# Performance work log

Hardware: AMD Instinct MI355X
Metric: run time of the kernel (lower is better)

## Reference

```python
import jax, jax.numpy as jnp
import numpy as np

Z, N, D_MODEL, HEADS = 2, 2048, 1024, 16
DK = D_MODEL // HEADS


def setup_inputs() -> dict:
    key = jax.random.key(0)
    ks = jax.random.split(key, 9)
    xavier = (6.0 / (DK + D_MODEL)) ** 0.5
    x = jax.random.normal(ks[0], (Z, N, D_MODEL), jnp.float32)
    mask = jax.random.randint(ks[1], (Z, N), 0, 2) > 0  # bool validity mask
    q_proj = jax.random.uniform(ks[2], (HEADS, D_MODEL, DK), jnp.float32, -xavier, xavier)
    k_proj = jax.random.uniform(ks[3], (HEADS, D_MODEL, DK), jnp.float32, -xavier, xavier)
    v_proj = jax.random.uniform(ks[4], (HEADS, D_MODEL, DK), jnp.float32, -xavier, xavier)
    q_bias = jnp.zeros((HEADS, DK), jnp.float32)
    k_bias = jnp.zeros((HEADS, DK), jnp.float32)
    v_bias = jnp.zeros((HEADS, DK), jnp.float32)
    lim = 1.0 / (D_MODEL ** 0.5)
    out_w = jax.random.uniform(ks[5], (D_MODEL, D_MODEL), jnp.float32, -lim, lim)  # torch Linear weight [out, in]
    return {"x": x, "mask": mask, "q_proj": q_proj, "k_proj": k_proj, "v_proj": v_proj,
            "q_bias": q_bias, "k_bias": k_bias, "v_bias": v_bias, "out_w": out_w}


def reference(x, mask, q_proj, k_proj, v_proj, q_bias, k_bias, v_bias, out_w):
    # Per-head QKV projections: [Z,N,Dm] x [H,Dm,Dk] -> [Z,H,N,Dk]
    Q = jnp.einsum('znd,hdk->zhnk', x, q_proj) + q_bias[None, :, None, :]
    K = jnp.einsum('znd,hdk->zhnk', x, k_proj) + k_bias[None, :, None, :]
    V = jnp.einsum('znd,hdk->zhnk', x, v_proj) + v_bias[None, :, None, :]
    scale = q_proj.shape[-1] ** -0.5
    # Dense equivalent of flash_attn_varlen over valid (unpadded) tokens:
    # mask invalid keys, softmax, then zero outputs at invalid query positions.
    scores = jnp.einsum('zhnk,zhmk->zhnm', Q, K) * scale
    neg = jnp.asarray(-1e9, scores.dtype)
    scores = jnp.where(mask[:, None, None, :], scores, neg)
    attn = jax.nn.softmax(scores, axis=-1)
    ctx = jnp.einsum('zhnm,zhmk->zhnk', attn, V)
    ctx = jnp.where(mask[:, None, :, None], ctx, jnp.zeros((), ctx.dtype))
    z, h, n, dk = ctx.shape
    out = ctx.transpose(0, 2, 1, 3).reshape(z, n, h * dk)  # [Z,N,Dm]
    return out @ out_w.T  # nn.Linear(d_model, d_model, bias=False)
```

## Files before the change

kernel.cpp:

```cpp
#include <hip/hip_runtime.h>
#include <stdint.h>

typedef __bf16 bf16_t;
typedef __bf16 bf16x8 __attribute__((ext_vector_type(8)));
typedef __bf16 bf16x4 __attribute__((ext_vector_type(4)));
typedef float f32x4 __attribute__((ext_vector_type(4)));

#define MFMA16(A, B, C) __builtin_amdgcn_mfma_f32_16x16x32_bf16(A, B, C, 0, 0, 0)

#if __has_builtin(__builtin_amdgcn_exp2f)
#define EXP2F(x) __builtin_amdgcn_exp2f(x)
#else
#define EXP2F(x) exp2f(x)
#endif

#define GLOAD_LDS16(g, l)                                                   \
  __builtin_amdgcn_global_load_lds(                                         \
      (const __attribute__((address_space(1))) void*)(g),                   \
      (__attribute__((address_space(3))) void*)(l), 16, 0, 0)

#define SL2E 0.18033688011112042f
#define VT_STRIDE 131072

__global__ __launch_bounds__(256) void convert_kernel(
    const float* __restrict__ x, const float* __restrict__ qw, const float* __restrict__ kw,
    const float* __restrict__ vw, const float* __restrict__ qb, const float* __restrict__ kb,
    const float* __restrict__ vb, const float* __restrict__ ow,
    bf16_t* __restrict__ xb, bf16_t* __restrict__ wqkv, bf16_t* __restrict__ wo,
    float* __restrict__ bias)
{
  const int bid = blockIdx.x, tid = threadIdx.x;
  if (bid < 768) {
    __shared__ float tile[64][65];
    int sh = bid >> 4, db = bid & 15;
    int sec = sh >> 4, h = sh & 15;
    int d0 = db * 64;
    const float* w = sec == 0 ? qw : (sec == 1 ? kw : vw);
    int dd = tid >> 2, kk0 = (tid & 3) * 16;
    const float* src = &w[((int64_t)h * 1024 + d0 + dd) * 64 + kk0];
#pragma unroll
    for (int j = 0; j < 4; j++) {
      float4 v = *(const float4*)&src[j * 4];
      tile[dd][kk0 + j * 4 + 0] = v.x;
      tile[dd][kk0 + j * 4 + 1] = v.y;
      tile[dd][kk0 + j * 4 + 2] = v.z;
      tile[dd][kk0 + j * 4 + 3] = v.w;
    }
    __syncthreads();
    int kk = tid >> 2, dd0 = (tid & 3) * 16;
    bf16x8 o0, o1;
#pragma unroll
    for (int j = 0; j < 8; j++) o0[j] = (bf16_t)tile[dd0 + j][kk];
#pragma unroll
    for (int j = 0; j < 8; j++) o1[j] = (bf16_t)tile[dd0 + 8 + j][kk];
    bf16_t* dst = &wqkv[(int64_t)(sh * 64 + kk) * 1024 + d0 + dd0];
    *(bf16x8*)dst = o0;
    *(bf16x8*)(dst + 8) = o1;
  } else if (bid < 2816) {
    int64_t base = ((int64_t)(bid - 768) * 256 + tid) * 8;
    float4 a = *(const float4*)&x[base];
    float4 b = *(const float4*)&x[base + 4];
    bf16x8 o = {(bf16_t)a.x, (bf16_t)a.y, (bf16_t)a.z, (bf16_t)a.w,
                (bf16_t)b.x, (bf16_t)b.y, (bf16_t)b.z, (bf16_t)b.w};
    *(bf16x8*)&xb[base] = o;
  } else if (bid < 3328) {
    int64_t base = ((int64_t)(bid - 2816) * 256 + tid) * 8;
    float4 a = *(const float4*)&ow[base];
    float4 b = *(const float4*)&ow[base + 4];
    bf16x8 o = {(bf16_t)a.x, (bf16_t)a.y, (bf16_t)a.z, (bf16_t)a.w,
                (bf16_t)b.x, (bf16_t)b.y, (bf16_t)b.z, (bf16_t)b.w};
    *(bf16x8*)&wo[base] = o;
  } else {
    for (int j = tid; j < 3072; j += 256) {
      int sec = j >> 10, c = j & 1023;
      const float* b = sec == 0 ? qb : (sec == 1 ? kb : vb);
      bias[j] = b[c];
    }
  }
}

template <int MODE, int TM>
__global__ __launch_bounds__(256) void gemm_kernel(
    const bf16_t* __restrict__ A, const bf16_t* __restrict__ Bt, const float* __restrict__ bias,
    bf16_t* __restrict__ qout, bf16_t* __restrict__ kout, bf16_t* __restrict__ vtout,
    float* __restrict__ fout, int Ndim)
{
  const int Kdim = 1024;
  const int MT = TM / 32;
  const int AS_SZ = TM * 64, BS_SZ = 128 * 64, BUF = AS_SZ + BS_SZ;
  __shared__ bf16_t smem[2 * (TM * 64 + 128 * 64)];

  const int tid = threadIdx.x;
  const int wave = tid >> 6, lane = tid & 63;
  const int l15 = lane & 15, quad = lane >> 4;
  const int wr = wave >> 1, wc = wave & 1;

  const int MB = 4096 / TM;
  const int GPX = MB / 8;
  const int xcd = blockIdx.x & 7, j = blockIdx.x >> 3;
  const int bm = (xcd * GPX + (j % GPX)) * TM;
  const int bn = (j / GPX) * 128;

  f32x4 acc[MT][4] = {};

  const int lr = lane >> 3;
  const int lc = (lane & 7) * 8;

  auto stage = [&](int b, int kk) {
    bf16_t* as = smem + b * BUF;
    bf16_t* bs = as + AS_SZ;
#pragma unroll
    for (int jj = 0; jj < MT; jj++) {
      int r = wave * (TM / 4) + jj * 8;
      GLOAD_LDS16(A + (int64_t)(bm + r + lr) * Kdim + kk + lc, &as[r * 64]);
    }
#pragma unroll
    for (int jj = 0; jj < 4; jj++) {
      int r = wave * 32 + jj * 8;
      GLOAD_LDS16(Bt + (int64_t)(bn + r + lr) * Kdim + kk + lc, &bs[r * 64]);
    }
  };

  stage(0, 0);
  for (int it = 0; it < 16; ++it) {
    int cur = it & 1;
    if (it < 15) {
      asm volatile("s_waitcnt lgkmcnt(0)\n\ts_barrier" ::: "memory");
      stage(cur ^ 1, (it + 1) * 64);
      asm volatile("s_waitcnt vmcnt(%0)" ::"i"(MT + 4) : "memory");
    } else {
      asm volatile("s_waitcnt vmcnt(0)" ::: "memory");
    }
    asm volatile("s_barrier" ::: "memory");
    const bf16_t* as = smem + cur * BUF;
    const bf16_t* bs = as + AS_SZ;
#pragma unroll
    for (int kc = 0; kc < 2; kc++) {
      bf16x8 af[MT], bfr[4];
#pragma unroll
      for (int mt = 0; mt < MT; mt++)
        af[mt] = *(const bf16x8*)&as[(wr * (TM / 2) + mt * 16 + l15) * 64 + kc * 32 + quad * 8];
#pragma unroll
      for (int nt = 0; nt < 4; nt++)
        bfr[nt] = *(const bf16x8*)&bs[(wc * 64 + nt * 16 + l15) * 64 + kc * 32 + quad * 8];
#pragma unroll
      for (int mt = 0; mt < MT; mt++)
#pragma unroll
        for (int nt = 0; nt < 4; nt++) acc[mt][nt] = MFMA16(af[mt], bfr[nt], acc[mt][nt]);
    }
  }

  if (MODE == 0 && bn >= 2048) {
    __syncthreads();
    bf16_t* Ct = smem;
    const int CTS = 136;
#pragma unroll
    for (int mt = 0; mt < MT; mt++) {
#pragma unroll
      for (int nt = 0; nt < 4; nt++) {
        int c = wc * 64 + nt * 16 + l15;
        int rw = wr * (TM / 2) + mt * 16 + quad * 4;
        bf16x4 pv;
#pragma unroll
        for (int r = 0; r < 4; r++) pv[r] = (bf16_t)(acc[mt][nt][r] + bias[bn + c]);
        *(bf16x4*)&Ct[c * CTS + rw] = pv;
      }
    }
    __syncthreads();
    int z = bm >> 11, n0 = bm & 2047;
    int colb = tid >> 4, nch = (tid & 15) * 8;
#pragma unroll
    for (int p = 0; p < 8; p++) {
      int c = p * 16 + colb;
      int hk = (bn + c) & 1023;
      int hh = hk >> 6, dk = hk & 63;
      int zh = z * 16 + hh;
      bf16x8 vv = *(const bf16x8*)&Ct[c * CTS + nch];
      *(bf16x8*)&vtout[(int64_t)zh * VT_STRIDE + dk * 2048 + n0 + nch] = vv;
    }
    return;
  }

#pragma unroll
  for (int mt = 0; mt < MT; mt++) {
#pragma unroll
    for (int nt = 0; nt < 4; nt++) {
#pragma unroll
      for (int r = 0; r < 4; r++) {
        int row = bm + wr * (TM / 2) + mt * 16 + quad * 4 + r;
        int col = bn + wc * 64 + nt * 16 + l15;
        float v = acc[mt][nt][r];
        if (MODE == 0) {
          v += bias[col];
          int sec = col >> 10, hk = col & 1023;
          int hh = hk >> 6, dk = hk & 63;
          int z = row >> 11, n = row & 2047;
          int zh = z * 16 + hh;
          if (sec == 0) {
            qout[(((int64_t)zh * 2048 + n) << 6) + dk] = (bf16_t)(v * SL2E);
          } else {
            kout[(((int64_t)zh * 2048 + n) << 6) + dk] = (bf16_t)v;
          }
        } else {
          fout[(int64_t)row * Ndim + col] = v;
        }
      }
    }
  }
}

__global__ __launch_bounds__(256, 2) void attn_kernel(
    const bf16_t* __restrict__ Q, const bf16_t* __restrict__ K, const bf16_t* __restrict__ Vt,
    const int* __restrict__ mask, bf16_t* __restrict__ ctx)
{
  __shared__ bf16_t Ks[2][64 * 64];
  __shared__ bf16_t Vs[2][64 * 64];
  __shared__ float Mkf[2048];
  __shared__ bf16_t Ps[4][2][16 * 72];

  const int tid = threadIdx.x;
  const int wave = tid >> 6, lane = tid & 63;
  const int l15 = lane & 15, quad = lane >> 4;
  const int bid = blockIdx.x;
  const int qt = bid & 15, zh = bid >> 4;
  const int z = zh >> 4, h = zh & 15;

  const bf16_t* Qb = Q + ((int64_t)zh * 2048 + qt * 128) * 64;
  const bf16_t* Kb = K + (int64_t)zh * 2048 * 64;
  const bf16_t* Vb = Vt + (int64_t)zh * VT_STRIDE;

  bf16x8 qf[2][2];
#pragma unroll
  for (int s = 0; s < 2; s++) {
    qf[s][0] = *(const bf16x8*)&Qb[(wave * 32 + s * 16 + l15) * 64 + quad * 8];
    qf[s][1] = *(const bf16x8*)&Qb[(wave * 32 + s * 16 + l15) * 64 + 32 + quad * 8];
  }

  {
    const int4* mp = (const int4*)(mask + z * 2048);
    for (int i = tid; i < 512; i += 256) {
      int4 m4 = mp[i];
      float4 f;
      f.x = m4.x ? 0.f : -1e30f;
      f.y = m4.y ? 0.f : -1e30f;
      f.z = m4.z ? 0.f : -1e30f;
      f.w = m4.w ? 0.f : -1e30f;
      *(float4*)&Mkf[i * 4] = f;
    }
  }

  const int slr = lane >> 3;
  const int scb = (lane & 7) ^ slr;
  auto stage = [&](int b, int kt2) {
#pragma unroll
    for (int c = 0; c < 2; c++) {
      int row = wave * 16 + c * 8;
      GLOAD_LDS16(Kb + (int64_t)(kt2 * 64 + row + slr) * 64 + scb * 8, &Ks[b][row * 64]);
      GLOAD_LDS16(Vb + (int64_t)(row + slr) * 2048 + kt2 * 64 + scb * 8, &Vs[b][row * 64]);
    }
  };

  stage(0, 0);

  float l_run[2] = {0.f, 0.f};
  f32x4 o[2][4] = {};
  const int sw = l15 & 7;

  for (int kt = 0; kt < 32; kt++) {
    int cur = kt & 1;
    asm volatile("s_waitcnt lgkmcnt(0)\n\ts_barrier" ::: "memory");
    if (kt < 31) {
      stage(cur ^ 1, kt + 1);
      asm volatile("s_waitcnt vmcnt(4)" ::: "memory");
    } else {
      asm volatile("s_waitcnt vmcnt(0)" ::: "memory");
    }
    asm volatile("s_barrier" ::: "memory");

    f32x4 minit[4];
    bf16x8 kf0[4], kf1[4], vf0[4], vf1[4];
#pragma unroll
    for (int mb = 0; mb < 4; mb++) {
      minit[mb] = *(const f32x4*)&Mkf[kt * 64 + mb * 16 + quad * 4];
      kf0[mb] = *(const bf16x8*)&Ks[cur][(mb * 16 + l15) * 64 + ((quad ^ sw) * 8)];
      kf1[mb] = *(const bf16x8*)&Ks[cur][(mb * 16 + l15) * 64 + (((quad + 4) ^ sw) * 8)];
      vf0[mb] = *(const bf16x8*)&Vs[cur][(mb * 16 + l15) * 64 + ((quad ^ sw) * 8)];
      vf1[mb] = *(const bf16x8*)&Vs[cur][(mb * 16 + l15) * 64 + (((quad + 4) ^ sw) * 8)];
    }

#pragma unroll
    for (int s = 0; s < 2; s++) {
      bf16_t* Psw = Ps[wave][s];
      float rs = 0.f;
#pragma unroll
      for (int mb = 0; mb < 4; mb++) {
        f32x4 t = minit[mb];
        t = MFMA16(kf0[mb], qf[s][0], t);
        t = MFMA16(kf1[mb], qf[s][1], t);
        bf16x4 pk;
#pragma unroll
        for (int r = 0; r < 4; r++) {
          float p = EXP2F(t[r]);
          rs += p;
          pk[r] = (bf16_t)p;
        }
        *(bf16x4*)&Psw[l15 * 72 + mb * 16 + quad * 4] = pk;
      }
      l_run[s] += rs;

      bf16x8 p0 = *(const bf16x8*)&Psw[l15 * 72 + quad * 8];
      bf16x8 p1 = *(const bf16x8*)&Psw[l15 * 72 + 32 + quad * 8];
#pragma unroll
      for (int nb = 0; nb < 4; nb++) {
        o[s][nb] = MFMA16(p0, vf0[nb], o[s][nb]);
        o[s][nb] = MFMA16(p1, vf1[nb], o[s][nb]);
      }
    }
  }

#pragma unroll
  for (int s = 0; s < 2; s++) {
    float l = l_run[s];
    l += __shfl_xor(l, 16);
    l += __shfl_xor(l, 32);
    float inv4[4];
#pragma unroll
    for (int r = 0; r < 4; r++) {
      int qrow = qt * 128 + wave * 32 + s * 16 + quad * 4 + r;
      float lv = __shfl(l, quad * 4 + r);
      int valid = mask[z * 2048 + qrow];
      inv4[r] = (valid && lv > 0.f) ? 1.0f / lv : 0.f;
    }
#pragma unroll
    for (int nb = 0; nb < 4; nb++) {
#pragma unroll
      for (int r = 0; r < 4; r++) {
        int qrow = qt * 128 + wave * 32 + s * 16 + quad * 4 + r;
        ctx[((int64_t)(z * 2048 + qrow)) * 1024 + h * 64 + nb * 16 + l15] =
            (bf16_t)(o[s][nb][r] * inv4[r]);
      }
    }
  }
}

extern "C" void kernel_launch(void* const* d_in, const int* in_sizes, int n_in,
                              void* d_out, int out_size, void* d_ws, size_t ws_size,
                              hipStream_t stream)
{
  (void)in_sizes; (void)n_in; (void)out_size; (void)ws_size;
  const float* x  = (const float*)d_in[0];
  const int* mask = (const int*)d_in[1];
  const float* qw = (const float*)d_in[2];
  const float* kw = (const float*)d_in[3];
  const float* vw = (const float*)d_in[4];
  const float* qb = (const float*)d_in[5];
  const float* kb = (const float*)d_in[6];
  const float* vb = (const float*)d_in[7];
  const float* ow = (const float*)d_in[8];
  float* out = (float*)d_out;

  bf16_t* xb   = (bf16_t*)d_ws;
  bf16_t* wqkv = xb + 4194304;
  bf16_t* wo   = wqkv + 3145728;
  float*  bias = (float*)(wo + 1048576);
  bf16_t* Qb   = (bf16_t*)(bias + 3072);
  bf16_t* Kb   = Qb + 4194304;
  bf16_t* Vtb  = Kb + 4194304;
  bf16_t* ctx  = Vtb + (int64_t)32 * VT_STRIDE;

  convert_kernel<<<3329, 256, 0, stream>>>(x, qw, kw, vw, qb, kb, vb, ow,
                                           xb, wqkv, wo, bias);
  gemm_kernel<0, 128><<<(4096 / 128) * (3072 / 128), 256, 0, stream>>>(
      xb, wqkv, bias, Qb, Kb, Vtb, nullptr, 3072);
  attn_kernel<<<2 * 16 * 16, 256, 0, stream>>>(Qb, Kb, Vtb, mask, ctx);
  gemm_kernel<1, 64><<<(4096 / 64) * (1024 / 128), 256, 0, stream>>>(
      ctx, wo, nullptr, nullptr, nullptr, nullptr, out, 1024);
}
```

Before: 197.8 us.

## Double attention query tile per block to reuse K/V fragments across more rows

Each attention block now processes 256 query rows (64 per wave, four 16-row subtiles) instead of 128, which halves the grid to 256 blocks. The inner loop is reordered so each K fragment and each V fragment read from LDS is used by all four subtiles, and the P tiles for all subtiles are staged in a larger shared buffer. This cuts LDS and global K/V traffic per query row. In exchange it uses more registers, drops the launch bound to one block per CU, and leaves fewer waves to hide latency.

```diff
diff --git a/kernel.cpp b/kernel.cpp
--- a/kernel.cpp
+++ b/kernel.cpp
@@ -209,31 +209,31 @@
   }
 }
 
-__global__ __launch_bounds__(256, 2) void attn_kernel(
+__global__ __launch_bounds__(256, 1) void attn_kernel(
     const bf16_t* __restrict__ Q, const bf16_t* __restrict__ K, const bf16_t* __restrict__ Vt,
     const int* __restrict__ mask, bf16_t* __restrict__ ctx)
 {
   __shared__ bf16_t Ks[2][64 * 64];
   __shared__ bf16_t Vs[2][64 * 64];
   __shared__ float Mkf[2048];
-  __shared__ bf16_t Ps[4][2][16 * 72];
+  __shared__ bf16_t Ps[4][4][16 * 72];
 
   const int tid = threadIdx.x;
   const int wave = tid >> 6, lane = tid & 63;
   const int l15 = lane & 15, quad = lane >> 4;
   const int bid = blockIdx.x;
-  const int qt = bid & 15, zh = bid >> 4;
+  const int qt = bid & 7, zh = bid >> 3;
   const int z = zh >> 4, h = zh & 15;
 
-  const bf16_t* Qb = Q + ((int64_t)zh * 2048 + qt * 128) * 64;
+  const bf16_t* Qb = Q + ((int64_t)zh * 2048 + qt * 256) * 64;
   const bf16_t* Kb = K + (int64_t)zh * 2048 * 64;
   const bf16_t* Vb = Vt + (int64_t)zh * VT_STRIDE;
 
-  bf16x8 qf[2][2];
-#pragma unroll
-  for (int s = 0; s < 2; s++) {
-    qf[s][0] = *(const bf16x8*)&Qb[(wave * 32 + s * 16 + l15) * 64 + quad * 8];
-    qf[s][1] = *(const bf16x8*)&Qb[(wave * 32 + s * 16 + l15) * 64 + 32 + quad * 8];
+  bf16x8 qf[4][2];
+#pragma unroll
+  for (int s = 0; s < 4; s++) {
+    qf[s][0] = *(const bf16x8*)&Qb[(wave * 64 + s * 16 + l15) * 64 + quad * 8];
+    qf[s][1] = *(const bf16x8*)&Qb[(wave * 64 + s * 16 + l15) * 64 + 32 + quad * 8];
   }
 
   {
@@ -262,8 +262,8 @@
 
   stage(0, 0);
 
-  float l_run[2] = {0.f, 0.f};
-  f32x4 o[2][4] = {};
+  float l_run[4] = {0.f, 0.f, 0.f, 0.f};
+  f32x4 o[4][4] = {};
   const int sw = l15 & 7;
 
   for (int kt = 0; kt < 32; kt++) {
@@ -277,56 +277,57 @@
     }
     asm volatile("s_barrier" ::: "memory");
 
-    f32x4 minit[4];
-    bf16x8 kf0[4], kf1[4], vf0[4], vf1[4];
 #pragma unroll
     for (int mb = 0; mb < 4; mb++) {
-      minit[mb] = *(const f32x4*)&Mkf[kt * 64 + mb * 16 + quad * 4];
-      kf0[mb] = *(const bf16x8*)&Ks[cur][(mb * 16 + l15) * 64 + ((quad ^ sw) * 8)];
-      kf1[mb] = *(const bf16x8*)&Ks[cur][(mb * 16 + l15) * 64 + (((quad + 4) ^ sw) * 8)];
-      vf0[mb] = *(const bf16x8*)&Vs[cur][(mb * 16 + l15) * 64 + ((quad ^ sw) * 8)];
-      vf1[mb] = *(const bf16x8*)&Vs[cur][(mb * 16 + l15) * 64 + (((quad + 4) ^ sw) * 8)];
-    }
-
-#pragma unroll
-    for (int s = 0; s < 2; s++) {
-      bf16_t* Psw = Ps[wave][s];
-      float rs = 0.f;
-#pragma unroll
-      for (int mb = 0; mb < 4; mb++) {
-        f32x4 t = minit[mb];
-        t = MFMA16(kf0[mb], qf[s][0], t);
-        t = MFMA16(kf1[mb], qf[s][1], t);
+      f32x4 minit = *(const f32x4*)&Mkf[kt * 64 + mb * 16 + quad * 4];
+      bf16x8 kf0 = *(const bf16x8*)&Ks[cur][(mb * 16 + l15) * 64 + ((quad ^ sw) * 8)];
+      bf16x8 kf1 = *(const bf16x8*)&Ks[cur][(mb * 16 + l15) * 64 + (((quad + 4) ^ sw) * 8)];
+#pragma unroll
+      for (int s = 0; s < 4; s++) {
+        f32x4 t = minit;
+        t = MFMA16(kf0, qf[s][0], t);
+        t = MFMA16(kf1, qf[s][1], t);
         bf16x4 pk;
+        float rs = 0.f;
 #pragma unroll
         for (int r = 0; r < 4; r++) {
           float p = EXP2F(t[r]);
           rs += p;
           pk[r] = (bf16_t)p;
         }
-        *(bf16x4*)&Psw[l15 * 72 + mb * 16 + quad * 4] = pk;
-      }
-      l_run[s] += rs;
-
-      bf16x8 p0 = *(const bf16x8*)&Psw[l15 * 72 + quad * 8];
-      bf16x8 p1 = *(const bf16x8*)&Psw[l15 * 72 + 32 + quad * 8];
-#pragma unroll
-      for (int nb = 0; nb < 4; nb++) {
-        o[s][nb] = MFMA16(p0, vf0[nb], o[s][nb]);
-        o[s][nb] = MFMA16(p1, vf1[nb], o[s][nb]);
-      }
-    }
-  }
-
-#pragma unroll
-  for (int s = 0; s < 2; s++) {
+        l_run[s] += rs;
+        *(bf16x4*)&Ps[wave][s][l15 * 72 + mb * 16 + quad * 4] = pk;
+      }
+    }
+
+    bf16x8 p0[4], p1[4];
+#pragma unroll
+    for (int s = 0; s < 4; s++) {
+      p0[s] = *(const bf16x8*)&Ps[wave][s][l15 * 72 + quad * 8];
+      p1[s] = *(const bf16x8*)&Ps[wave][s][l15 * 72 + 32 + quad * 8];
+    }
+
+#pragma unroll
+    for (int nb = 0; nb < 4; nb++) {
+      bf16x8 vf0 = *(const bf16x8*)&Vs[cur][(nb * 16 + l15) * 64 + ((quad ^ sw) * 8)];
+      bf16x8 vf1 = *(const bf16x8*)&Vs[cur][(nb * 16 + l15) * 64 + (((quad + 4) ^ sw) * 8)];
+#pragma unroll
+      for (int s = 0; s < 4; s++) {
+        o[s][nb] = MFMA16(p0[s], vf0, o[s][nb]);
+        o[s][nb] = MFMA16(p1[s], vf1, o[s][nb]);
+      }
+    }
+  }
+
+#pragma unroll
+  for (int s = 0; s < 4; s++) {
     float l = l_run[s];
     l += __shfl_xor(l, 16);
     l += __shfl_xor(l, 32);
     float inv4[4];
 #pragma unroll
     for (int r = 0; r < 4; r++) {
-      int qrow = qt * 128 + wave * 32 + s * 16 + quad * 4 + r;
+      int qrow = qt * 256 + wave * 64 + s * 16 + quad * 4 + r;
       float lv = __shfl(l, quad * 4 + r);
       int valid = mask[z * 2048 + qrow];
       inv4[r] = (valid && lv > 0.f) ? 1.0f / lv : 0.f;
@@ -335,7 +336,7 @@
     for (int nb = 0; nb < 4; nb++) {
 #pragma unroll
       for (int r = 0; r < 4; r++) {
-        int qrow = qt * 128 + wave * 32 + s * 16 + quad * 4 + r;
+        int qrow = qt * 256 + wave * 64 + s * 16 + quad * 4 + r;
         ctx[((int64_t)(z * 2048 + qrow)) * 1024 + h * 64 + nb * 16 + l15] =
             (bf16_t)(o[s][nb][r] * inv4[r]);
       }
@@ -372,7 +373,7 @@
                                            xb, wqkv, wo, bias);
   gemm_kernel<0, 128><<<(4096 / 128) * (3072 / 128), 256, 0, stream>>>(
       xb, wqkv, bias, Qb, Kb, Vtb, nullptr, 3072);
-  attn_kernel<<<2 * 16 * 16, 256, 0, stream>>>(Qb, Kb, Vtb, mask, ctx);
+  attn_kernel<<<32 * 8, 256, 0, stream>>>(Qb, Kb, Vtb, mask, ctx);
   gemm_kernel<1, 64><<<(4096 / 64) * (1024 / 128), 256, 0, stream>>>(
       ctx, wo, nullptr, nullptr, nullptr, nullptr, out, 1024);
 }
```

New measurement: 215.7 us. +9.1%, slower.
